# Kernel optimization log

Measured on AMD Instinct MI355X. Metric: run time of the kernel, lower is better.

## Reference

```python
import jax, jax.numpy as jnp
import numpy as np

B, E, R, HSZ, HEADS, PROP, RTOKS = 16, 400, 624, 512, 4, 2, 40
N = E + R            # nodes per graph = entities + relations
DFF = HSZ * HEADS    # Block FFN width (l1: hsz -> hsz*heads)


def setup_inputs() -> dict:
    key = jax.random.key(0)
    ks = jax.random.split(key, 12)
    ents = jax.random.normal(ks[0], (B, E, HSZ), jnp.float32)
    rels = jax.random.randint(ks[1], (B, R), 0, RTOKS)
    adj = jax.random.randint(ks[2], (B, N, N), 0, 2)
    # self-loops so no softmax row is fully masked
    d = jnp.arange(N)
    adj = adj.at[:, d, d].set(1)
    renc = jax.random.normal(ks[3], (RTOKS, HSZ)) * (2.0 / (RTOKS + HSZ)) ** 0.5

    def lin(k, fi, fo):  # weights stored (in, out): y = x @ W + b
        return jax.random.normal(k, (PROP, fi, fo)) * (1.0 / fi) ** 0.5

    Wq = lin(ks[4], HSZ, HSZ)
    Wk = lin(ks[5], HSZ, HSZ)
    Wv = lin(ks[6], HSZ, HSZ)
    l1_w = lin(ks[7], HSZ, DFF)
    l1_b = jnp.zeros((PROP, DFF))
    l2_w = lin(ks[8], DFF, HSZ)
    l2_b = jnp.zeros((PROP, HSZ))
    ln1_s = jnp.ones((PROP, HSZ)); ln1_b = jnp.zeros((PROP, HSZ))
    ln2_s = jnp.ones((PROP, HSZ)); ln2_b = jnp.zeros((PROP, HSZ))
    prelu_a = jnp.full((PROP, DFF), 0.25)
    return dict(ents=ents, rels=rels, adj=adj, renc=renc, Wq=Wq, Wk=Wk, Wv=Wv,
                l1_w=l1_w, l1_b=l1_b, l2_w=l2_w, l2_b=l2_b,
                ln1_s=ln1_s, ln1_b=ln1_b, ln2_s=ln2_s, ln2_b=ln2_b,
                prelu_a=prelu_a)


def _layer_norm(x, s, b, eps=1e-5):
    mu = jnp.mean(x, -1, keepdims=True)
    var = jnp.mean((x - mu) ** 2, -1, keepdims=True)
    return (x - mu) * jax.lax.rsqrt(var + eps) * s + b


def _mha(q, kv, adj, Wq, Wk, Wv):
    # GraphWriter MultiHeadAttention: split heads by contiguous chunks,
    # scale by sqrt(key_dim)=sqrt(HSZ), mask where adj==0, residual += query.
    dk = HSZ // HEADS
    Q = (q @ Wq).reshape(B, N, HEADS, dk)
    K = (kv @ Wk).reshape(B, N, HEADS, dk)
    V = (kv @ Wv).reshape(B, N, HEADS, dk)
    scores = jnp.einsum('bnhd,bmhd->bhnm', Q, K) / np.sqrt(HSZ).astype(np.float32)
    scores = jnp.where((adj == 0)[:, None, :, :], -jnp.inf, scores)
    attn = jax.nn.softmax(scores, axis=-1)
    out = jnp.einsum('bhnm,bmhd->bnhd', attn, V).reshape(B, N, HSZ)
    return out + q


def _encode(ents, rels, adj, renc, Wq, Wk, Wv, l1_w, l1_b, l2_w, l2_b,
            ln1_s, ln1_b, ln2_s, ln2_b, prelu_a):
    x = jnp.concatenate([ents, renc[rels]], axis=1)  # (B, N, HSZ)
    for j in range(PROP):  # fixed small number of propagation Blocks
        kv = jax.lax.stop_gradient(x)  # dense path wraps kv in torch.tensor(requires_grad=False)
        out = _mha(x, kv, adj, Wq[j], Wk[j], Wv[j])
        t = _layer_norm(out, ln1_s[j], ln1_b[j])
        h = t @ l1_w[j] + l1_b[j]
        h = jnp.maximum(h, 0) + prelu_a[j] * jnp.minimum(h, 0)  # PReLU
        h = h @ l2_w[j] + l2_b[j]  # dropout p=0 (eval)
        x = _layer_norm(h + t, ln2_s[j], ln2_b[j])
    return x


def reference(ents, rels, adj, renc, Wq, Wk, Wv, l1_w, l1_b, l2_w, l2_b,
              ln1_s, ln1_b, ln2_s, ln2_b, prelu_a):
    nodes = _encode(ents, rels, adj, renc, Wq, Wk, Wv, l1_w, l1_b, l2_w, l2_b,
                    ln1_s, ln1_b, ln2_s, ln2_b, prelu_a)
    glob = nodes[:, E]  # node at index ent_lens[i] (first relation node)
    node_mask = jnp.ones((B, N), dtype=bool)  # ent_lens uniform -> all valid
    return glob, nodes, node_mask
```

## Files before the change

### kernel.cpp

```cpp
#include <hip/hip_runtime.h>
#include <hip/hip_bf16.h>

typedef __bf16 bf16;
typedef __attribute__((ext_vector_type(8))) bf16 bf16x8;
typedef __attribute__((ext_vector_type(4))) float f32x4;

constexpr int B_   = 16;
constexpr int E_   = 400;
constexpr int R_   = 624;
constexpr int N_   = 1024;
constexpr int HSZ_ = 512;
constexpr int DFF_ = 2048;
constexpr int M_   = B_ * N_;

__device__ __forceinline__ void glds16(const void* g, void* l) {
    __builtin_amdgcn_global_load_lds((const __attribute__((address_space(1))) void*)g,
                                     (__attribute__((address_space(3))) void*)l,
                                     16, 0, 0);
}

__global__ __launch_bounds__(256) void transpose_f32_bf16(const float* __restrict__ in,
                                                          bf16* __restrict__ out,
                                                          int rows, int cols) {
    __shared__ float tile[32][33];
    int c0 = blockIdx.x * 32, r0 = blockIdx.y * 32;
    int tx = threadIdx.x, ty = threadIdx.y;
    #pragma unroll
    for (int i = 0; i < 32; i += 8)
        tile[ty + i][tx] = in[(size_t)(r0 + ty + i) * cols + (c0 + tx)];
    __syncthreads();
    #pragma unroll
    for (int i = 0; i < 32; i += 8)
        out[(size_t)(c0 + ty + i) * rows + (r0 + tx)] = (bf16)tile[tx][ty + i];
}

__global__ __launch_bounds__(256) void pack_adj(const int* __restrict__ adj,
                                                unsigned* __restrict__ adjw) {
    int gid  = blockIdx.x * 4 + (threadIdx.x >> 6);
    int lane = threadIdx.x & 63;
    int w64  = gid & 15;
    int bn   = gid >> 4;
    int v = adj[(size_t)bn * N_ + w64 * 64 + lane];
    unsigned long long mask = __ballot(v != 0);
    if (lane == 0)  adjw[bn * 32 + w64 * 2]     = (unsigned)mask;
    if (lane == 32) adjw[bn * 32 + w64 * 2 + 1] = (unsigned)(mask >> 32);
}

__global__ __launch_bounds__(256) void build_x(const float* __restrict__ ents,
                                               const int* __restrict__ rels,
                                               const float* __restrict__ renc,
                                               bf16* __restrict__ x) {
    int idx  = blockIdx.x * 256 + threadIdx.x;
    int col8 = (idx & 63) * 8;
    int row  = idx >> 6;
    int b = row >> 10, n = row & 1023;
    const float* src;
    if (n < E_) src = ents + ((size_t)(b * E_ + n)) * HSZ_ + col8;
    else {
        int rt = rels[b * R_ + (n - E_)];
        src = renc + (size_t)rt * HSZ_ + col8;
    }
    float4 a = *(const float4*)src;
    float4 c = *(const float4*)(src + 4);
    bf16x8 v;
    v[0] = (bf16)a.x; v[1] = (bf16)a.y; v[2] = (bf16)a.z; v[3] = (bf16)a.w;
    v[4] = (bf16)c.x; v[5] = (bf16)c.y; v[6] = (bf16)c.z; v[7] = (bf16)c.w;
    *(bf16x8*)(x + (size_t)row * HSZ_ + col8) = v;
}

template <int MODE>
__global__ __launch_bounds__(256) void gemm_bt(const bf16* __restrict__ A,
                                               const bf16* __restrict__ Bt,
                                               const float* __restrict__ biasF,
                                               const float* __restrict__ alphaF,
                                               const bf16* __restrict__ extraB,
                                               bf16* __restrict__ outB,
                                               bf16* __restrict__ outB2,
                                               bf16* __restrict__ outB3,
                                               float* __restrict__ outF,
                                               int Nn, int Kk) {
    __shared__ bf16 As[128][64];
    __shared__ bf16 Bs[128][64];
    int n0 = blockIdx.x * 128, m0 = blockIdx.y * 128;
    int t = threadIdx.x;
    int lane = t & 63, r = lane & 15, quad = lane >> 4;
    int w = t >> 6;
    int wm = w >> 1, wn = w & 1;
    f32x4 acc[4][4];
    #pragma unroll
    for (int mt = 0; mt < 4; mt++)
        #pragma unroll
        for (int nt = 0; nt < 4; nt++) acc[mt][nt] = (f32x4){0.f, 0.f, 0.f, 0.f};

    for (int k0 = 0; k0 < Kk; k0 += 64) {
        #pragma unroll
        for (int i = 0; i < 4; i++) {
            int e = i * 256 + t;
            int row = e >> 3, c8 = (e & 7) * 8;
            glds16(&A[(size_t)(m0 + row) * Kk + k0 + c8], &As[row][c8]);
            glds16(&Bt[(size_t)(n0 + row) * Kk + k0 + c8], &Bs[row][c8]);
        }
        __syncthreads();
        #pragma unroll
        for (int kk = 0; kk < 64; kk += 32) {
            bf16x8 af[4], bfr[4];
            #pragma unroll
            for (int mt = 0; mt < 4; mt++)
                af[mt] = *(const bf16x8*)&As[wm * 64 + mt * 16 + r][kk + quad * 8];
            #pragma unroll
            for (int nt = 0; nt < 4; nt++)
                bfr[nt] = *(const bf16x8*)&Bs[wn * 64 + nt * 16 + r][kk + quad * 8];
            #pragma unroll
            for (int mt = 0; mt < 4; mt++)
                #pragma unroll
                for (int nt = 0; nt < 4; nt++)
                    acc[mt][nt] = __builtin_amdgcn_mfma_f32_16x16x32_bf16(af[mt], bfr[nt], acc[mt][nt], 0, 0, 0);
        }
        __syncthreads();
    }
    #pragma unroll
    for (int mt = 0; mt < 4; mt++) {
        #pragma unroll
        for (int nt = 0; nt < 4; nt++) {
            #pragma unroll
            for (int i = 0; i < 4; i++) {
                int rg = m0 + wm * 64 + mt * 16 + quad * 4 + i;
                int cg = n0 + wn * 64 + nt * 16 + r;
                float v = acc[mt][nt][i];
                if (MODE == 0) {
                    outB[(size_t)rg * Nn + cg] = (bf16)v;
                } else if (MODE == 1) {
                    int bb = rg >> 10, n = rg & 1023;
                    outB[(size_t)(bb * HSZ_ + cg) * N_ + n] = (bf16)v;
                } else if (MODE == 2) {
                    v += biasF[cg];
                    float a = alphaF[cg];
                    v = v > 0.f ? v : a * v;
                    outB[(size_t)rg * Nn + cg] = (bf16)v;
                } else if (MODE == 3) {
                    v += biasF[cg] + (float)extraB[(size_t)rg * Nn + cg];
                    outF[(size_t)rg * Nn + cg] = v;
                } else {
                    if (cg < 512) {
                        outB[(size_t)rg * HSZ_ + cg] = (bf16)v;
                    } else if (cg < 1024) {
                        outB2[(size_t)rg * HSZ_ + (cg - 512)] = (bf16)v;
                    } else {
                        int bb = rg >> 10, n = rg & 1023;
                        outB3[(size_t)(bb * HSZ_ + (cg - 1024)) * N_ + n] = (bf16)v;
                    }
                }
            }
        }
    }
}

__global__ __launch_bounds__(256) void attn_fused(const bf16* __restrict__ Q,
                                                  const bf16* __restrict__ K,
                                                  const bf16* __restrict__ Vt,
                                                  const unsigned* __restrict__ adjw,
                                                  const bf16* __restrict__ xb,
                                                  float* __restrict__ tpre) {
    int blk = blockIdx.x;
    int gr = blk & 7;
    int qb = (blk >> 3) & 7;
    int gq = blk >> 6;
    int g = gq * 8 + gr;
    int b = g >> 2, h = g & 3;

    int tid = threadIdx.x;
    int w = tid >> 6, lane = tid & 63;
    int r = lane & 15, quad = lane >> 4;
    int n0 = qb * 128 + w * 32;

    __shared__ bf16 Ks[64][136];
    __shared__ bf16 Vs[128][72];
    __shared__ bf16 plds[4][32][68];

    int kRow = tid >> 4, kCol = (tid & 15) * 8;
    int vRow = tid >> 3, vCol = (tid & 7) * 8;
    const bf16* Kg = K + (size_t)(b * N_) * HSZ_ + h * 128 + (size_t)kRow * HSZ_ + kCol;
    const bf16* Vg = Vt + (size_t)(b * HSZ_ + h * 128 + vRow) * N_ + vCol;
    bf16* KsP = &Ks[kRow][kCol];
    bf16* VsP = &Vs[vRow][vCol];

    uint4 kp0, kp1, kp2, kp3, vp0, vp1, vp2, vp3;

#define ATTN_ISSUE(it_) do {                                                      \
        const bf16* kg_ = Kg + (size_t)(it_) * 64 * HSZ_;                         \
        const bf16* vg_ = Vg + (it_) * 64;                                        \
        kp0 = *(const uint4*)(kg_);                                               \
        kp1 = *(const uint4*)(kg_ + 16 * HSZ_);                                   \
        kp2 = *(const uint4*)(kg_ + 32 * HSZ_);                                   \
        kp3 = *(const uint4*)(kg_ + 48 * HSZ_);                                   \
        vp0 = *(const uint4*)(vg_);                                               \
        vp1 = *(const uint4*)(vg_ + 32 * N_);                                     \
        vp2 = *(const uint4*)(vg_ + 64 * N_);                                     \
        vp3 = *(const uint4*)(vg_ + 96 * N_);                                     \
    } while (0)

#define ATTN_COMMIT() do {                                                        \
        *(uint4*)(KsP)            = kp0;                                          \
        *(uint4*)(KsP + 16 * 136) = kp1;                                          \
        *(uint4*)(KsP + 32 * 136) = kp2;                                          \
        *(uint4*)(KsP + 48 * 136) = kp3;                                          \
        *(uint4*)(VsP)            = vp0;                                          \
        *(uint4*)(VsP + 32 * 72)  = vp1;                                          \
        *(uint4*)(VsP + 64 * 72)  = vp2;                                          \
        *(uint4*)(VsP + 96 * 72)  = vp3;                                          \
    } while (0)

    bf16x8 qf[2][4];
    #pragma unroll
    for (int mt = 0; mt < 2; mt++) {
        const bf16* qbase = Q + ((size_t)(b * N_ + n0 + mt * 16 + r)) * HSZ_ + h * 128;
        #pragma unroll
        for (int kc = 0; kc < 4; kc++) qf[mt][kc] = *(const bf16x8*)(qbase + kc * 32 + quad * 8);
    }

    f32x4 accv[2][8];
    #pragma unroll
    for (int mt = 0; mt < 2; mt++)
        #pragma unroll
        for (int dt = 0; dt < 8; dt++) accv[mt][dt] = (f32x4){0.f, 0.f, 0.f, 0.f};
    float tl[2][4] = {{0.f, 0.f, 0.f, 0.f}, {0.f, 0.f, 0.f, 0.f}};
    const float scale = 0.04419417382415922f;
    const float SHIFT = 12.0f;

    ATTN_ISSUE(0);
    for (int it = 0; it < 16; it++) {
        __syncthreads();
        ATTN_COMMIT();
        __syncthreads();
        if (it + 1 < 16) ATTN_ISSUE(it + 1);

        f32x4 cg[2][4];
        #pragma unroll
        for (int mt = 0; mt < 2; mt++)
            #pragma unroll
            for (int gk = 0; gk < 4; gk++) cg[mt][gk] = (f32x4){0.f, 0.f, 0.f, 0.f};
        __builtin_amdgcn_s_setprio(1);
        #pragma unroll
        for (int gk = 0; gk < 4; gk++)
            #pragma unroll
            for (int kc = 0; kc < 4; kc++) {
                bf16x8 kf = *(const bf16x8*)&Ks[gk * 16 + r][kc * 32 + quad * 8];
                cg[0][gk] = __builtin_amdgcn_mfma_f32_16x16x32_bf16(qf[0][kc], kf, cg[0][gk], 0, 0, 0);
                cg[1][gk] = __builtin_amdgcn_mfma_f32_16x16x32_bf16(qf[1][kc], kf, cg[1][gk], 0, 0, 0);
            }
        __builtin_amdgcn_s_setprio(0);
        #pragma unroll
        for (int mt = 0; mt < 2; mt++)
            #pragma unroll
            for (int i = 0; i < 4; i++) {
                int row_l = mt * 16 + quad * 4 + i;
                int row_g = n0 + row_l;
                const unsigned* aw = &adjw[((size_t)(b << 10) + row_g) * 32 + it * 2];
                unsigned wb0 = aw[0], wb1 = aw[1];
                float p0 = ((wb0 >> r) & 1u)        ? __expf(cg[mt][0][i] * scale - SHIFT) : 0.f;
                float p1 = ((wb0 >> (16 + r)) & 1u) ? __expf(cg[mt][1][i] * scale - SHIFT) : 0.f;
                float p2 = ((wb1 >> r) & 1u)        ? __expf(cg[mt][2][i] * scale - SHIFT) : 0.f;
                float p3 = ((wb1 >> (16 + r)) & 1u) ? __expf(cg[mt][3][i] * scale - SHIFT) : 0.f;
                tl[mt][i] += p0 + p1 + p2 + p3;
                plds[w][row_l][r]      = (bf16)p0;
                plds[w][row_l][16 + r] = (bf16)p1;
                plds[w][row_l][32 + r] = (bf16)p2;
                plds[w][row_l][48 + r] = (bf16)p3;
            }

        bf16x8 pf00 = *(const bf16x8*)&plds[w][r][quad * 8];
        bf16x8 pf01 = *(const bf16x8*)&plds[w][r][32 + quad * 8];
        bf16x8 pf10 = *(const bf16x8*)&plds[w][16 + r][quad * 8];
        bf16x8 pf11 = *(const bf16x8*)&plds[w][16 + r][32 + quad * 8];
        __builtin_amdgcn_s_setprio(1);
        #pragma unroll
        for (int dt = 0; dt < 8; dt++) {
            bf16x8 v0 = *(const bf16x8*)&Vs[dt * 16 + r][quad * 8];
            bf16x8 v1 = *(const bf16x8*)&Vs[dt * 16 + r][32 + quad * 8];
            accv[0][dt] = __builtin_amdgcn_mfma_f32_16x16x32_bf16(pf00, v0, accv[0][dt], 0, 0, 0);
            accv[0][dt] = __builtin_amdgcn_mfma_f32_16x16x32_bf16(pf01, v1, accv[0][dt], 0, 0, 0);
            accv[1][dt] = __builtin_amdgcn_mfma_f32_16x16x32_bf16(pf10, v0, accv[1][dt], 0, 0, 0);
            accv[1][dt] = __builtin_amdgcn_mfma_f32_16x16x32_bf16(pf11, v1, accv[1][dt], 0, 0, 0);
        }
        __builtin_amdgcn_s_setprio(0);
    }
#undef ATTN_ISSUE
#undef ATTN_COMMIT

    #pragma unroll
    for (int mt = 0; mt < 2; mt++)
        #pragma unroll
        for (int i = 0; i < 4; i++) {
            float l = tl[mt][i];
            #pragma unroll
            for (int d = 1; d < 16; d <<= 1) l += __shfl_xor(l, d, 64);
            float inv_l = 1.0f / fmaxf(l, 1e-30f);
            #pragma unroll
            for (int dt = 0; dt < 8; dt++) {
                int row = n0 + mt * 16 + quad * 4 + i;
                int col = h * 128 + dt * 16 + r;
                size_t idx = ((size_t)(b * N_ + row)) * HSZ_ + col;
                tpre[idx] = accv[mt][dt][i] * inv_l + (float)xb[idx];
            }
        }
}

__global__ __launch_bounds__(256) void lnorm_k(const float* __restrict__ in,
                                               const float* __restrict__ sc,
                                               const float* __restrict__ bi,
                                               bf16* __restrict__ out) {
    int row = blockIdx.x * 4 + (threadIdx.x >> 6);
    int lane = threadIdx.x & 63;
    const float* rp = in + (size_t)row * HSZ_;
    float4 a = *(const float4*)(rp + lane * 4);
    float4 b = *(const float4*)(rp + 256 + lane * 4);
    float sum = a.x + a.y + a.z + a.w + b.x + b.y + b.z + b.w;
    float sq  = a.x*a.x + a.y*a.y + a.z*a.z + a.w*a.w
              + b.x*b.x + b.y*b.y + b.z*b.z + b.w*b.w;
    #pragma unroll
    for (int d = 1; d < 64; d <<= 1) {
        sum += __shfl_xor(sum, d, 64);
        sq  += __shfl_xor(sq,  d, 64);
    }
    float mu = sum * (1.0f / HSZ_);
    float varv = fmaxf(sq * (1.0f / HSZ_) - mu * mu, 0.f);
    float rs = rsqrtf(varv + 1e-5f);
    bf16* op = out + (size_t)row * HSZ_;
    int c0 = lane * 4;
    float va[4] = {a.x, a.y, a.z, a.w}, vb[4] = {b.x, b.y, b.z, b.w};
    #pragma unroll
    for (int k = 0; k < 4; k++) {
        op[c0 + k]       = (bf16)(((va[k] - mu) * rs) * sc[c0 + k] + bi[c0 + k]);
        op[c0 + 256 + k] = (bf16)(((vb[k] - mu) * rs) * sc[c0 + 256 + k] + bi[c0 + 256 + k]);
    }
}

__global__ __launch_bounds__(256) void write_out(const bf16* __restrict__ x,
                                                 float* __restrict__ out) {
    size_t tid = (size_t)blockIdx.x * 256 + threadIdx.x;
    if (tid < (size_t)B_ * HSZ_) {
        int b = (int)(tid >> 9), c = (int)(tid & 511);
        out[tid] = (float)x[((size_t)(b * N_ + E_)) * HSZ_ + c];
    } else if (tid < (size_t)B_ * HSZ_ + (size_t)B_ * N_ * HSZ_) {
        out[tid] = (float)x[tid - B_ * HSZ_];
    } else {
        out[tid] = 1.0f;
    }
}

extern "C" void kernel_launch(void* const* d_in, const int* in_sizes, int n_in,
                              void* d_out, int out_size, void* d_ws, size_t ws_size,
                              hipStream_t stream) {
    const float* ents = (const float*)d_in[0];
    const int*   rels = (const int*)d_in[1];
    const int*   adj  = (const int*)d_in[2];
    const float* renc = (const float*)d_in[3];
    const float* Wq   = (const float*)d_in[4];
    const float* Wk   = (const float*)d_in[5];
    const float* Wv   = (const float*)d_in[6];
    const float* l1w  = (const float*)d_in[7];
    const float* l1b  = (const float*)d_in[8];
    const float* l2w  = (const float*)d_in[9];
    const float* l2b  = (const float*)d_in[10];
    const float* ln1s = (const float*)d_in[11];
    const float* ln1b = (const float*)d_in[12];
    const float* ln2s = (const float*)d_in[13];
    const float* ln2b = (const float*)d_in[14];
    const float* pa   = (const float*)d_in[15];

    char* ws = (char*)d_ws;
    size_t o = 0;
    auto alloc = [&](size_t bytes) { void* p = ws + o; o += bytes; return p; };
    bf16*     WqkvT  = (bf16*)alloc(3145728);
    bf16*     L1T    = (bf16*)alloc(4194304);
    bf16*     L2T    = (bf16*)alloc(4194304);
    unsigned* adjw   = (unsigned*)alloc(2097152);
    bf16*     xb     = (bf16*)alloc(16777216);
    bf16*     Qb     = (bf16*)alloc(16777216);
    bf16*     Kb     = (bf16*)alloc(16777216);
    bf16*     Vt     = (bf16*)alloc(16777216);
    bf16*     tb     = (bf16*)alloc(16777216);
    bf16*     hb     = (bf16*)alloc(67108864);
    float*    f32buf = (float*)alloc(33554432);
    if (o > ws_size) return;

    dim3 t32(32, 8);
    for (int j = 0; j < 2; j++) {
        transpose_f32_bf16<<<dim3(16, 16), t32, 0, stream>>>(Wq  + j * 262144,  WqkvT + j * 786432,          512, 512);
        transpose_f32_bf16<<<dim3(16, 16), t32, 0, stream>>>(Wk  + j * 262144,  WqkvT + j * 786432 + 262144, 512, 512);
        transpose_f32_bf16<<<dim3(16, 16), t32, 0, stream>>>(Wv  + j * 262144,  WqkvT + j * 786432 + 524288, 512, 512);
        transpose_f32_bf16<<<dim3(64, 16), t32, 0, stream>>>(l1w + j * 1048576, L1T + j * 1048576, 512, 2048);
        transpose_f32_bf16<<<dim3(16, 64), t32, 0, stream>>>(l2w + j * 1048576, L2T + j * 1048576, 2048, 512);
    }
    pack_adj<<<65536, 256, 0, stream>>>(adj, adjw);
    build_x<<<4096, 256, 0, stream>>>(ents, rels, renc, xb);

    for (int j = 0; j < 2; j++) {
        gemm_bt<4><<<dim3(12, 128), 256, 0, stream>>>(xb, WqkvT + j * 786432, nullptr, nullptr, nullptr,
                                                      Qb, Kb, Vt, nullptr, 1536, 512);
        attn_fused<<<512, 256, 0, stream>>>(Qb, Kb, Vt, adjw, xb, f32buf);
        lnorm_k<<<4096, 256, 0, stream>>>(f32buf, ln1s + j * 512, ln1b + j * 512, tb);
        gemm_bt<2><<<dim3(16, 128), 256, 0, stream>>>(tb, L1T + j * 1048576, l1b + j * 2048, pa + j * 2048,
                                                      nullptr, hb, nullptr, nullptr, nullptr, 2048, 512);
        gemm_bt<3><<<dim3(4, 128), 256, 0, stream>>>(hb, L2T + j * 1048576, l2b + j * 512, nullptr,
                                                     tb, nullptr, nullptr, nullptr, f32buf, 512, 2048);
        lnorm_k<<<4096, 256, 0, stream>>>(f32buf, ln2s + j * 512, ln2b + j * 512, xb);
    }
    write_out<<<32864, 256, 0, stream>>>(xb, (float*)d_out);
}
```

Before: 727.6 us.

## Double-buffer LDS tiles in bf16 GEMM to overlap loads with MFMA

Doubles the shared-memory A/B tiles and prefetches the next K-tile with global_load_lds while the current tile is consumed by MFMA, so each iteration needs one barrier instead of two. Load addresses are also precomputed once per thread. This targets the exposed global-load latency in the GEMM main loop, at the cost of twice the LDS (64KB per block), which may reduce occupancy. Correctness depends on the single barrier covering both the completion of the prefetch and the end of reads from the other buffer.

```diff
diff --git a/kernel.cpp b/kernel.cpp
--- a/kernel.cpp
+++ b/kernel.cpp
@@ -79,37 +79,51 @@
                                                bf16* __restrict__ outB3,
                                                float* __restrict__ outF,
                                                int Nn, int Kk) {
-    __shared__ bf16 As[128][64];
-    __shared__ bf16 Bs[128][64];
+    __shared__ bf16 As[2][128][64];
+    __shared__ bf16 Bs[2][128][64];
     int n0 = blockIdx.x * 128, m0 = blockIdx.y * 128;
     int t = threadIdx.x;
     int lane = t & 63, r = lane & 15, quad = lane >> 4;
     int w = t >> 6;
     int wm = w >> 1, wn = w & 1;
+
+    int sRow = t >> 3, sCol = (t & 7) * 8;
+    const bf16* Ag = A  + (size_t)(m0 + sRow) * Kk + sCol;
+    const bf16* Bg = Bt + (size_t)(n0 + sRow) * Kk + sCol;
+
+#define G_STAGE(p_, k0_) do {                                          \
+        glds16(Ag + (k0_),              &As[p_][sRow     ][sCol]);     \
+        glds16(Ag + 32 * Kk + (k0_),    &As[p_][sRow + 32][sCol]);     \
+        glds16(Ag + 64 * Kk + (k0_),    &As[p_][sRow + 64][sCol]);     \
+        glds16(Ag + 96 * Kk + (k0_),    &As[p_][sRow + 96][sCol]);     \
+        glds16(Bg + (k0_),              &Bs[p_][sRow     ][sCol]);     \
+        glds16(Bg + 32 * Kk + (k0_),    &Bs[p_][sRow + 32][sCol]);     \
+        glds16(Bg + 64 * Kk + (k0_),    &Bs[p_][sRow + 64][sCol]);     \
+        glds16(Bg + 96 * Kk + (k0_),    &Bs[p_][sRow + 96][sCol]);     \
+    } while (0)
+
     f32x4 acc[4][4];
     #pragma unroll
     for (int mt = 0; mt < 4; mt++)
         #pragma unroll
         for (int nt = 0; nt < 4; nt++) acc[mt][nt] = (f32x4){0.f, 0.f, 0.f, 0.f};
 
-    for (int k0 = 0; k0 < Kk; k0 += 64) {
-        #pragma unroll
-        for (int i = 0; i < 4; i++) {
-            int e = i * 256 + t;
-            int row = e >> 3, c8 = (e & 7) * 8;
-            glds16(&A[(size_t)(m0 + row) * Kk + k0 + c8], &As[row][c8]);
-            glds16(&Bt[(size_t)(n0 + row) * Kk + k0 + c8], &Bs[row][c8]);
-        }
-        __syncthreads();
+    G_STAGE(0, 0);
+    __syncthreads();
+
+    int ntiles = Kk >> 6;
+    for (int tt = 0; tt < ntiles; tt++) {
+        int p = tt & 1;
+        if (tt + 1 < ntiles) G_STAGE(p ^ 1, (tt + 1) * 64);
         #pragma unroll
         for (int kk = 0; kk < 64; kk += 32) {
             bf16x8 af[4], bfr[4];
             #pragma unroll
             for (int mt = 0; mt < 4; mt++)
-                af[mt] = *(const bf16x8*)&As[wm * 64 + mt * 16 + r][kk + quad * 8];
+                af[mt] = *(const bf16x8*)&As[p][wm * 64 + mt * 16 + r][kk + quad * 8];
             #pragma unroll
             for (int nt = 0; nt < 4; nt++)
-                bfr[nt] = *(const bf16x8*)&Bs[wn * 64 + nt * 16 + r][kk + quad * 8];
+                bfr[nt] = *(const bf16x8*)&Bs[p][wn * 64 + nt * 16 + r][kk + quad * 8];
             #pragma unroll
             for (int mt = 0; mt < 4; mt++)
                 #pragma unroll
@@ -118,6 +132,8 @@
         }
         __syncthreads();
     }
+#undef G_STAGE
+
     #pragma unroll
     for (int mt = 0; mt < 4; mt++) {
         #pragma unroll
```

Result: no change. 734.9 us (+1.0%).

## Swizzle GEMM shared-memory tiles and remap workgroups across XCDs

Applied to the files above, without the earlier changes.

The GEMM now stores each 16-byte column chunk of the A and B tiles at an XOR-permuted LDS position, chosen by row, so MFMA fragment reads avoid LDS bank conflicts. The global load addresses are precomputed once per thread rather than recomputed every k-step. Workgroup IDs are also remapped so that consecutive tiles land on the same XCD, aiming for better L2 reuse. The remap assumes the workgroup count is divisible by 8; otherwise some tiles could be skipped or duplicated.

```diff
diff --git a/kernel.cpp b/kernel.cpp
--- a/kernel.cpp
+++ b/kernel.cpp
@@ -81,35 +81,58 @@
                                                int Nn, int Kk) {
     __shared__ bf16 As[128][64];
     __shared__ bf16 Bs[128][64];
-    int n0 = blockIdx.x * 128, m0 = blockIdx.y * 128;
+
+    int nwg = gridDim.x * gridDim.y;
+    int bid = blockIdx.y * gridDim.x + blockIdx.x;
+    int q = nwg >> 3;
+    int ng = (bid & 7) * q + (bid >> 3);
+    int bx = ng % gridDim.x, by = ng / gridDim.x;
+
+    int n0 = bx * 128, m0 = by * 128;
     int t = threadIdx.x;
     int lane = t & 63, r = lane & 15, quad = lane >> 4;
     int w = t >> 6;
     int wm = w >> 1, wn = w & 1;
+
+    int sRow = t >> 3;
+    int xr   = sRow & 7;
+    int sColL = (t & 7) * 8;
+    int sColG = ((t & 7) ^ xr) * 8;
+    const bf16* Ag = A  + (size_t)(m0 + sRow) * Kk + sColG;
+    const bf16* Bg = Bt + (size_t)(n0 + sRow) * Kk + sColG;
+
+#define G_STAGE(k0_) do {                                          \
+        glds16(Ag + (k0_),           &As[sRow     ][sColL]);       \
+        glds16(Ag + 32 * Kk + (k0_), &As[sRow + 32][sColL]);       \
+        glds16(Ag + 64 * Kk + (k0_), &As[sRow + 64][sColL]);       \
+        glds16(Ag + 96 * Kk + (k0_), &As[sRow + 96][sColL]);       \
+        glds16(Bg + (k0_),           &Bs[sRow     ][sColL]);       \
+        glds16(Bg + 32 * Kk + (k0_), &Bs[sRow + 32][sColL]);       \
+        glds16(Bg + 64 * Kk + (k0_), &Bs[sRow + 64][sColL]);       \
+        glds16(Bg + 96 * Kk + (k0_), &Bs[sRow + 96][sColL]);       \
+    } while (0)
+
     f32x4 acc[4][4];
     #pragma unroll
     for (int mt = 0; mt < 4; mt++)
         #pragma unroll
         for (int nt = 0; nt < 4; nt++) acc[mt][nt] = (f32x4){0.f, 0.f, 0.f, 0.f};
 
+    int xa = r & 7;
+
     for (int k0 = 0; k0 < Kk; k0 += 64) {
-        #pragma unroll
-        for (int i = 0; i < 4; i++) {
-            int e = i * 256 + t;
-            int row = e >> 3, c8 = (e & 7) * 8;
-            glds16(&A[(size_t)(m0 + row) * Kk + k0 + c8], &As[row][c8]);
-            glds16(&Bt[(size_t)(n0 + row) * Kk + k0 + c8], &Bs[row][c8]);
-        }
+        G_STAGE(k0);
         __syncthreads();
         #pragma unroll
         for (int kk = 0; kk < 64; kk += 32) {
+            int pc = (((kk >> 3) + quad) ^ xa) * 8;
             bf16x8 af[4], bfr[4];
             #pragma unroll
             for (int mt = 0; mt < 4; mt++)
-                af[mt] = *(const bf16x8*)&As[wm * 64 + mt * 16 + r][kk + quad * 8];
+                af[mt] = *(const bf16x8*)&As[wm * 64 + mt * 16 + r][pc];
             #pragma unroll
             for (int nt = 0; nt < 4; nt++)
-                bfr[nt] = *(const bf16x8*)&Bs[wn * 64 + nt * 16 + r][kk + quad * 8];
+                bfr[nt] = *(const bf16x8*)&Bs[wn * 64 + nt * 16 + r][pc];
             #pragma unroll
             for (int mt = 0; mt < 4; mt++)
                 #pragma unroll
@@ -118,6 +141,8 @@
         }
         __syncthreads();
     }
+#undef G_STAGE
+
     #pragma unroll
     for (int mt = 0; mt < 4; mt++) {
         #pragma unroll
```

Result: faster. 698.1 us (-4.1%).
